# Kernel optimization log

Measured on AMD Instinct MI355X. Metric: run time of the kernel, lower is better.

## Reference

```python
import jax, jax.numpy as jnp
import numpy as np

N = 50000        # nodes
E = 800000       # edges
F_IN = 32        # float features (x also carries 1 trailing cell-id column)
CELL_DIM = 16
NUM_CELLS = 854
C = 64           # out_channels
H0, H1 = 2, 1    # heads schedule for num_layers=2 -> [2, 1]
D_IN = F_IN + CELL_DIM  # 48, GAT input dim after cell embedding concat
NEG_SLOPE = 0.2  # PyG GATConv default negative_slope


def setup_inputs() -> dict:
    key = jax.random.key(0)
    ks = jax.random.split(key, 14)
    base = jax.random.normal(ks[0], (N, F_IN), jnp.float32)
    cell_ids = jax.random.randint(ks[1], (N,), 0, NUM_CELLS)
    x = jnp.concatenate([base, cell_ids.astype(jnp.float32)[:, None]], axis=1)
    edge_index = jax.random.randint(ks[2], (2, E), 0, N, dtype=jnp.int32)
    s = lambda f: 1.0 / np.sqrt(f)
    emb = jax.random.normal(ks[3], (NUM_CELLS, CELL_DIM), jnp.float32)
    W0 = jax.random.normal(ks[4], (D_IN, H0 * C), jnp.float32) * s(D_IN)
    a_src0 = jax.random.normal(ks[5], (H0, C), jnp.float32) * s(C)
    a_dst0 = jax.random.normal(ks[6], (H0, C), jnp.float32) * s(C)
    b0 = jnp.zeros((C,), jnp.float32)
    ln_g = jnp.ones((C,), jnp.float32)
    ln_b = jnp.zeros((C,), jnp.float32)
    W1 = jax.random.normal(ks[7], (C, H1 * C), jnp.float32) * s(C)
    a_src1 = jax.random.normal(ks[8], (H1, C), jnp.float32) * s(C)
    a_dst1 = jax.random.normal(ks[9], (H1, C), jnp.float32) * s(C)
    b1 = jnp.zeros((C,), jnp.float32)
    return {"x": x, "edge_index": edge_index, "emb": emb,
            "W0": W0, "a_src0": a_src0, "a_dst0": a_dst0, "b0": b0,
            "ln_g": ln_g, "ln_b": ln_b,
            "W1": W1, "a_src1": a_src1, "a_dst1": a_dst1, "b1": b1}


def gat_layer(h_in, src, dst, W, a_src, a_dst, b, heads):
    # h_in: [N, D]; src/dst: [E'] (self-loops already appended)
    h = (h_in @ W).reshape(N, heads, C)                 # [N, H, C]
    alpha_s = jnp.einsum('nhc,hc->nh', h, a_src)        # [N, H]
    alpha_d = jnp.einsum('nhc,hc->nh', h, a_dst)
    e = jax.nn.leaky_relu(alpha_s[src] + alpha_d[dst], NEG_SLOPE)  # [E', H]
    # segment softmax over incoming edges of each dst node
    m = jax.ops.segment_max(e, dst, num_segments=N)     # [N, H]
    ex = jnp.exp(e - m[dst])
    denom = jax.ops.segment_sum(ex, dst, num_segments=N)
    alpha = ex / denom[dst]                             # [E', H]
    msg = h[src] * alpha[:, :, None]                    # [E', H, C]
    out = jax.ops.segment_sum(msg, dst, num_segments=N) # [N, H, C]
    return out.mean(axis=1) + b                         # concat=False -> mean over heads


def layer_norm(x, g, b):
    mu = x.mean(-1, keepdims=True)
    var = ((x - mu) ** 2).mean(-1, keepdims=True)
    return (x - mu) * jax.lax.rsqrt(var + 1e-5) * g + b


def reference(x, edge_index, emb, W0, a_src0, a_dst0, b0, ln_g, ln_b,
              W1, a_src1, a_dst1, b1):
    base = x[:, :-1]
    cell_ids = x[:, -1].astype(jnp.int32)
    h = jnp.concatenate([base, emb[cell_ids]], axis=1)  # [N, 48]
    # add self-loops (PyG GATConv default add_self_loops=True)
    loop = jnp.arange(N, dtype=edge_index.dtype)
    src = jnp.concatenate([edge_index[0], loop])
    dst = jnp.concatenate([edge_index[1], loop])
    h = gat_layer(h, src, dst, W0, a_src0, a_dst0, b0, H0)
    h = jax.nn.elu(layer_norm(h, ln_g, ln_b))           # dropout is identity at eval
    h = gat_layer(h, src, dst, W1, a_src1, a_dst1, b1, H1)
    return h
```

## Files before the change

kernel.cpp:

```cpp
#include <hip/hip_runtime.h>
#include <hip/hip_bf16.h>

#define N_NODES 50000
#define N_EDGES 800000
#define E_TOT 850000
#define F_IN 32
#define CELL_DIM 16
#define D_IN 48
#define X_STRIDE 33
#define NUM_CELLS 854
#define NEG_SLOPE 0.2f
#define NODE0_BLOCKS 1024
#define MERGE_BLOCKS 1563
#define EDGE_BLOCKS 3125
#define NXCD 8
#define BWX 16
#define W 24
#define NP 12

typedef unsigned int uint;
typedef unsigned short ushort;

static __device__ __forceinline__ uint f2b(float f) {
  uint x = __float_as_uint(f);
  return (x + 0x7fffu + ((x >> 16) & 1u)) >> 16;
}
static __device__ __forceinline__ float b2f_lo(uint w) { return __uint_as_float(w << 16); }
static __device__ __forceinline__ float b2f_hi(uint w) { return __uint_as_float(w & 0xffff0000u); }
static __device__ __forceinline__ float lrelu(float e) { return fmaxf(e, NEG_SLOPE * e); }


__global__ __launch_bounds__(256) void k_nb(const float* __restrict__ x,
                                            const float* __restrict__ emb,
                                            const float* __restrict__ W0,
                                            const float* __restrict__ asrc,
                                            const float* __restrict__ adst,
                                            const int* __restrict__ ei,
                                            ushort* __restrict__ h0u,
                                            float* __restrict__ as0, float* __restrict__ ad0,
                                            int* __restrict__ cnt, ushort* __restrict__ bkt) {
  int tid = threadIdx.x;
  if (blockIdx.x >= NODE0_BLOCKS) {
    int e = (blockIdx.x - NODE0_BLOCKS) * 256 + tid;
    if (e < N_EDGES) {
      uint xcc;
      asm volatile("s_getreg_b32 %0, hwreg(HW_REG_XCC_ID)" : "=s"(xcc));
      xcc &= (NXCD - 1);
      int s = ei[e], d = ei[N_EDGES + e];
      int p = atomicAdd(&cnt[xcc * N_NODES + d], 1);
      if (p < BWX) bkt[(xcc * N_NODES + d) * BWX + p] = (ushort)s;
    }
    return;
  }
  __shared__ float hin[8][48];
  int lane = tid & 63, wid = tid >> 6;
  int h = wid & 1;
  int q = wid >> 1;
  float w0r[D_IN];
#pragma unroll
  for (int k = 0; k < D_IN; ++k) w0r[k] = W0[k * 128 + h * 64 + lane];
  float av_s = asrc[h * 64 + lane], av_d = adst[h * 64 + lane];

  for (int g = blockIdx.x; g < N_NODES / 8; g += NODE0_BLOCKS) {
    int nb = g * 8;
#pragma unroll
    for (int j = 0; j < 2; ++j) {
      int loc = 2 * wid + j;
      int n = nb + loc;
      float t = 0.f;
      if (lane < 33) t = x[n * X_STRIDE + lane];
      int cid = (int)__shfl(t, 32, 64);
      cid = cid < 0 ? 0 : (cid >= NUM_CELLS ? NUM_CELLS - 1 : cid);
      if (lane >= 32 && lane < 48) t = emb[cid * CELL_DIM + (lane - 32)];
      if (lane < 48) hin[loc][lane] = t;
    }
    __syncthreads();
#pragma unroll
    for (int j = 0; j < 4; ++j) {
      int loc = 4 * q + j;
      int n = nb + loc;
      const float4* hp = (const float4*)hin[loc];
      float acc = 0.f;
#pragma unroll
      for (int k4 = 0; k4 < 12; ++k4) {
        float4 hh = hp[k4];
        acc = fmaf(hh.x, w0r[4 * k4 + 0], acc);
        acc = fmaf(hh.y, w0r[4 * k4 + 1], acc);
        acc = fmaf(hh.z, w0r[4 * k4 + 2], acc);
        acc = fmaf(hh.w, w0r[4 * k4 + 3], acc);
      }
      h0u[(n * 64 + lane) * 2 + h] = (ushort)f2b(acc);
      float sa = acc * av_s, sd = acc * av_d;
#pragma unroll
      for (int o = 32; o >= 1; o >>= 1) {
        sa += __shfl_xor(sa, o, 64);
        sd += __shfl_xor(sd, o, 64);
      }
      if (lane == 0) {
        as0[n * 2 + h] = sa;
        ad0[n * 2 + h] = sd;
      }
    }
    __syncthreads();
  }
}


__global__ __launch_bounds__(256) void k_merge(const int* __restrict__ cnt,
                                               const ushort* __restrict__ bkt,
                                               const float2* __restrict__ as0v,
                                               const float2* __restrict__ ad0v,
                                               int* __restrict__ galloc,
                                               int2* __restrict__ meta,
                                               ushort* __restrict__ srcs,
                                               uint* __restrict__ wts) {
  __shared__ int gpre[32];
  __shared__ int bbase;
  int tid = threadIdx.x;
  int grp = tid >> 3;
  int n = blockIdx.x * 32 + grp;
  bool alive = (n < N_NODES);
  int xg = tid & 7;
  int cx = alive ? min(cnt[xg * N_NODES + n], BWX) : 0;
  int sc = cx;
#pragma unroll
  for (int o = 1; o < 8; o <<= 1) {
    int t = __shfl_up(sc, o, 64);
    if ((tid & 7) >= o) sc += t;
  }
  int total = __shfl(sc, (tid & 63) | 7, 64);
  int items = alive ? total + 1 : 0;
  if (xg == 7) gpre[grp] = items;
  __syncthreads();
  if (tid < 32) {
    int v = gpre[tid];
    int s = v;
#pragma unroll
    for (int o = 1; o < 32; o <<= 1) {
      int t = __shfl_up(s, o, 64);
      if (tid >= o) s += t;
    }
    gpre[tid] = s - v;
    if (tid == 31) bbase = atomicAdd(galloc, s);
  }
  __syncthreads();
  if (!alive) return;
  int start = bbase + gpre[grp];
  int base = start + (sc - cx);
  float2 ad = ad0v[n];
  const ushort* src = bkt + (xg * N_NODES + n) * BWX;
  for (int k = 0; k < cx; ++k) {
    uint s = src[k];
    float2 a = as0v[s];
    uint wp = f2b(__expf(lrelu(a.x + ad.x))) | (f2b(__expf(lrelu(a.y + ad.y))) << 16);
    srcs[base + k] = (ushort)s;
    wts[base + k] = wp;
  }
  if (xg == 7) {
    float2 a = as0v[n];
    uint wp = f2b(__expf(lrelu(a.x + ad.x))) | (f2b(__expf(lrelu(a.y + ad.y))) << 16);
    srcs[start + total] = (ushort)n;
    wts[start + total] = wp;
    meta[n] = make_int2(start, items);
  }
}


__global__ __launch_bounds__(256) void k_agg0(const int2* __restrict__ meta,
                                              const ushort* __restrict__ srcs,
                                              const uint* __restrict__ wts,
                                              const uint* __restrict__ h0p,
                                              const float* __restrict__ b0,
                                              const float* __restrict__ lng,
                                              const float* __restrict__ lnb,
                                              const float* __restrict__ W1,
                                              const float* __restrict__ asrc1,
                                              const float* __restrict__ adst1,
                                              ushort* __restrict__ h1b,
                                              float* __restrict__ as1, float* __restrict__ ad1) {
  __shared__ uint gbuf[4][W * 64];
  __shared__ float yb[4][64];
  int tid = threadIdx.x;
  int lane = tid & 63, wl = tid >> 6;
  int n = blockIdx.x * 4 + wl;
  int2 mt = meta[n];
  int i0 = mt.x, i1 = mt.x + mt.y;
  float acc0 = 0.f, acc1 = 0.f, den0 = 0.f, den1 = 0.f;
  uint* gb = gbuf[wl];

  for (int w0 = i0; w0 < i1; w0 += W) {
    int idx = w0 + lane;
    uint s = 0u, wy = 0u;
    if (lane < W && idx < i1) {
      s = (uint)srcs[idx];
      wy = wts[idx];
    }
#pragma unroll
    for (int j = 0; j < W; ++j) {
      uint sx = (uint)__builtin_amdgcn_readlane((int)s, j);
      __builtin_amdgcn_global_load_lds((const uint*)(h0p + sx * 64u + (uint)lane),
                                       gb + j * 64, 4, 0, 0);
    }
    asm volatile("s_waitcnt vmcnt(0)" ::: "memory");
    __builtin_amdgcn_sched_barrier(0);
#pragma unroll
    for (int j = 0; j < W; ++j) {
      uint wyj = (uint)__builtin_amdgcn_readlane((int)wy, j);
      uint h = gb[j * 64 + lane];
      float w;
      w = b2f_lo(wyj); acc0 += w * b2f_lo(h); den0 += w;
      w = b2f_hi(wyj); acc1 += w * b2f_hi(h); den1 += w;
    }
    asm volatile("s_waitcnt lgkmcnt(0)" ::: "memory");
    __builtin_amdgcn_sched_barrier(0);
  }

  float v = 0.5f * (acc0 / den0 + acc1 / den1) + b0[lane];
  float mu = v;
#pragma unroll
  for (int o = 32; o >= 1; o >>= 1) mu += __shfl_xor(mu, o, 64);
  mu *= (1.0f / 64.0f);
  float d = v - mu;
  float vr = d * d;
#pragma unroll
  for (int o = 32; o >= 1; o >>= 1) vr += __shfl_xor(vr, o, 64);
  vr *= (1.0f / 64.0f);
  float y = d * rsqrtf(vr + 1e-5f) * lng[lane] + lnb[lane];
  y = y > 0.f ? y : expm1f(y);
  yb[wl][lane] = y;
  const float4* yp = (const float4*)yb[wl];
  float q0 = 0.f, q1 = 0.f, q2 = 0.f, q3 = 0.f;
#pragma unroll
  for (int k4 = 0; k4 < 16; ++k4) {
    float4 yy = yp[k4];
    q0 = fmaf(yy.x, W1[(4 * k4 + 0) * 64 + lane], q0);
    q1 = fmaf(yy.y, W1[(4 * k4 + 1) * 64 + lane], q1);
    q2 = fmaf(yy.z, W1[(4 * k4 + 2) * 64 + lane], q2);
    q3 = fmaf(yy.w, W1[(4 * k4 + 3) * 64 + lane], q3);
  }
  float h1v = (q0 + q1) + (q2 + q3);
  h1b[n * 64 + lane] = (ushort)f2b(h1v);
  float sa = h1v * asrc1[lane];
  float sdv = h1v * adst1[lane];
#pragma unroll
  for (int o = 32; o >= 1; o >>= 1) {
    sa += __shfl_xor(sa, o, 64);
    sdv += __shfl_xor(sdv, o, 64);
  }
  if (lane == 0) {
    as1[n] = sa;
    ad1[n] = sdv;
  }
}


__global__ __launch_bounds__(256) void k_agg1(const int2* __restrict__ meta,
                                              const ushort* __restrict__ srcs,
                                              const ushort* __restrict__ h1b,
                                              const float* __restrict__ as1,
                                              const float* __restrict__ ad1,
                                              const float* __restrict__ b1,
                                              float* __restrict__ out) {
  __shared__ uint gbuf[4][NP * 64];
  int tid = threadIdx.x;
  int lane = tid & 63, wl = tid >> 6;
  int n = blockIdx.x * 4 + wl;
  int2 mt = meta[n];
  int i0 = mt.x, i1 = mt.x + mt.y;
  float adv = ad1[n];
  float acc = 0.f, den = 0.f;
  uint* gb = gbuf[wl];
  const ushort* gbs = (const ushort*)gb;
  uint hl = lane & 31;
  int half = lane >> 5;

  for (int w0 = i0; w0 < i1; w0 += W) {
    int idx = w0 + lane;
    uint s = 0u;
    float wv = 0.f;
    if (lane < W && idx < i1) {
      s = (uint)srcs[idx];
      wv = __expf(lrelu(as1[s] + adv));
    }
#pragma unroll
    for (int j = 0; j < NP; ++j) {
      uint sxA = (uint)__builtin_amdgcn_readlane((int)s, 2 * j);
      uint sxB = (uint)__builtin_amdgcn_readlane((int)s, 2 * j + 1);
      uint sx2 = half ? sxB : sxA;
      __builtin_amdgcn_global_load_lds((const uint*)(h1b + sx2 * 64u) + hl,
                                       gb + j * 64, 4, 0, 0);
    }
    asm volatile("s_waitcnt vmcnt(0)" ::: "memory");
    __builtin_amdgcn_sched_barrier(0);
#pragma unroll
    for (int j = 0; j < NP; ++j) {
      float wA = __uint_as_float(
          (uint)__builtin_amdgcn_readlane((int)__float_as_uint(wv), 2 * j));
      float wB = __uint_as_float(
          (uint)__builtin_amdgcn_readlane((int)__float_as_uint(wv), 2 * j + 1));
      uint hA = (uint)gbs[j * 128 + lane];
      uint hB = (uint)gbs[j * 128 + 64 + lane];
      acc = fmaf(wA, __uint_as_float(hA << 16), acc);
      den += wA;
      acc = fmaf(wB, __uint_as_float(hB << 16), acc);
      den += wB;
    }
    asm volatile("s_waitcnt lgkmcnt(0)" ::: "memory");
    __builtin_amdgcn_sched_barrier(0);
  }
  out[n * 64 + lane] = acc / den + b1[lane];
}


extern "C" void kernel_launch(void* const* d_in, const int* in_sizes, int n_in,
                              void* d_out, int out_size, void* d_ws, size_t ws_size,
                              hipStream_t stream) {
  const float* x    = (const float*)d_in[0];
  const int*   ei   = (const int*)d_in[1];
  const float* emb  = (const float*)d_in[2];
  const float* W0   = (const float*)d_in[3];
  const float* as0w = (const float*)d_in[4];
  const float* ad0w = (const float*)d_in[5];
  const float* b0   = (const float*)d_in[6];
  const float* lng  = (const float*)d_in[7];
  const float* lnb  = (const float*)d_in[8];
  const float* W1   = (const float*)d_in[9];
  const float* as1w = (const float*)d_in[10];
  const float* ad1w = (const float*)d_in[11];
  const float* b1   = (const float*)d_in[12];
  float* out = (float*)d_out;

  ushort* bkt    = (ushort*)d_ws;
  ushort* h1b    = (ushort*)d_ws;
  int*    cnt    = (int*)((char*)d_ws + (size_t)NXCD * N_NODES * BWX * 2);
  int*    galloc = cnt + NXCD * N_NODES;
  float*  as1    = (float*)cnt;
  float*  ad1    = as1 + N_NODES;
  int2*   meta   = (int2*)(galloc + 2);
  ushort* srcs   = (ushort*)(meta + N_NODES);
  uint*   wts    = (uint*)(srcs + E_TOT);
  float*  as0    = (float*)(wts + E_TOT);
  float*  ad0    = as0 + N_NODES * 2;
  uint*   h0p    = (uint*)(ad0 + N_NODES * 2);

  hipMemsetAsync(cnt, 0, (NXCD * N_NODES + 2) * sizeof(int), stream);
  k_nb<<<NODE0_BLOCKS + EDGE_BLOCKS, 256, 0, stream>>>(x, emb, W0, as0w, ad0w, ei,
                                                       (ushort*)h0p, as0, ad0, cnt, bkt);
  k_merge<<<MERGE_BLOCKS, 256, 0, stream>>>(cnt, bkt, (const float2*)as0,
                                            (const float2*)ad0, galloc, meta, srcs, wts);
  k_agg0<<<N_NODES / 4, 256, 0, stream>>>(meta, srcs, wts, h0p, b0, lng, lnb, W1,
                                          as1w, ad1w, h1b, as1, ad1);
  k_agg1<<<N_NODES / 4, 256, 0, stream>>>(meta, srcs, h1b, as1, ad1, b1, out);
}
```

Measured before the change: 240.0 us.

## Precompute layer-1 edge weights in separate edge-parallel kernel packed with source ids

Adds a k_merge output of per-edge destination ids and a new edge-parallel kernel k_wts1. That kernel computes the layer-1 attention weight exp(lrelu(as1[s]+ad1[d])) for every edge and packs it as bf16 with the 16-bit source id into one 32-bit record. k_agg1 then reads a single packed record per edge instead of a source id plus a dependent as1 gather and exp. This moves latency-bound dependent gathers off the aggregation critical path into a fully parallel pass. The cost is an extra kernel launch, an extra edge array write and read, and layer-1 weights rounded to bf16.

```diff
diff --git a/kernel.cpp b/kernel.cpp
--- a/kernel.cpp
+++ b/kernel.cpp
@@ -13,6 +13,7 @@
 #define NODE0_BLOCKS 1024
 #define MERGE_BLOCKS 1563
 #define EDGE_BLOCKS 3125
+#define WTS1_BLOCKS 3321
 #define NXCD 8
 #define BWX 16
 #define W 24
@@ -113,6 +114,7 @@
                                                int* __restrict__ galloc,
                                                int2* __restrict__ meta,
                                                ushort* __restrict__ srcs,
+                                               ushort* __restrict__ dsts,
                                                uint* __restrict__ wts) {
   __shared__ int gpre[32];
   __shared__ int bbase;
@@ -154,12 +156,14 @@
     float2 a = as0v[s];
     uint wp = f2b(__expf(lrelu(a.x + ad.x))) | (f2b(__expf(lrelu(a.y + ad.y))) << 16);
     srcs[base + k] = (ushort)s;
+    dsts[base + k] = (ushort)n;
     wts[base + k] = wp;
   }
   if (xg == 7) {
     float2 a = as0v[n];
     uint wp = f2b(__expf(lrelu(a.x + ad.x))) | (f2b(__expf(lrelu(a.y + ad.y))) << 16);
     srcs[start + total] = (ushort)n;
+    dsts[start + total] = (ushort)n;
     wts[start + total] = wp;
     meta[n] = make_int2(start, items);
   }
@@ -254,11 +258,22 @@
 }
 
 
-__global__ __launch_bounds__(256) void k_agg1(const int2* __restrict__ meta,
-                                              const ushort* __restrict__ srcs,
-                                              const ushort* __restrict__ h1b,
+__global__ __launch_bounds__(256) void k_wts1(const ushort* __restrict__ srcs,
+                                              const ushort* __restrict__ dsts,
                                               const float* __restrict__ as1,
                                               const float* __restrict__ ad1,
+                                              uint* __restrict__ rec32) {
+  int e = blockIdx.x * 256 + threadIdx.x;
+  if (e >= E_TOT) return;
+  uint s = srcs[e], d = dsts[e];
+  float w = __expf(lrelu(as1[s] + ad1[d]));
+  rec32[e] = s | (f2b(w) << 16);
+}
+
+
+__global__ __launch_bounds__(256) void k_agg1(const int2* __restrict__ meta,
+                                              const uint* __restrict__ rec32,
+                                              const ushort* __restrict__ h1b,
                                               const float* __restrict__ b1,
                                               float* __restrict__ out) {
   __shared__ uint gbuf[4][NP * 64];
@@ -267,7 +282,6 @@
   int n = blockIdx.x * 4 + wl;
   int2 mt = meta[n];
   int i0 = mt.x, i1 = mt.x + mt.y;
-  float adv = ad1[n];
   float acc = 0.f, den = 0.f;
   uint* gb = gbuf[wl];
   const ushort* gbs = (const ushort*)gb;
@@ -276,17 +290,13 @@
 
   for (int w0 = i0; w0 < i1; w0 += W) {
     int idx = w0 + lane;
-    uint s = 0u;
-    float wv = 0.f;
-    if (lane < W && idx < i1) {
-      s = (uint)srcs[idx];
-      wv = __expf(lrelu(as1[s] + adv));
-    }
+    uint rec = 0u;
+    if (lane < W && idx < i1) rec = rec32[idx];
 #pragma unroll
     for (int j = 0; j < NP; ++j) {
-      uint sxA = (uint)__builtin_amdgcn_readlane((int)s, 2 * j);
-      uint sxB = (uint)__builtin_amdgcn_readlane((int)s, 2 * j + 1);
-      uint sx2 = half ? sxB : sxA;
+      uint rA = (uint)__builtin_amdgcn_readlane((int)rec, 2 * j);
+      uint rB = (uint)__builtin_amdgcn_readlane((int)rec, 2 * j + 1);
+      uint sx2 = (half ? rB : rA) & 0xffffu;
       __builtin_amdgcn_global_load_lds((const uint*)(h1b + sx2 * 64u) + hl,
                                        gb + j * 64, 4, 0, 0);
     }
@@ -294,10 +304,8 @@
     __builtin_amdgcn_sched_barrier(0);
 #pragma unroll
     for (int j = 0; j < NP; ++j) {
-      float wA = __uint_as_float(
-          (uint)__builtin_amdgcn_readlane((int)__float_as_uint(wv), 2 * j));
-      float wB = __uint_as_float(
-          (uint)__builtin_amdgcn_readlane((int)__float_as_uint(wv), 2 * j + 1));
+      float wA = b2f_hi((uint)__builtin_amdgcn_readlane((int)rec, 2 * j));
+      float wB = b2f_hi((uint)__builtin_amdgcn_readlane((int)rec, 2 * j + 1));
       uint hA = (uint)gbs[j * 128 + lane];
       uint hB = (uint)gbs[j * 128 + 64 + lane];
       acc = fmaf(wA, __uint_as_float(hA << 16), acc);
@@ -332,13 +340,15 @@
 
   ushort* bkt    = (ushort*)d_ws;
   ushort* h1b    = (ushort*)d_ws;
+  uint*   rec32  = (uint*)((char*)d_ws + (size_t)N_NODES * 64 * 2);
   int*    cnt    = (int*)((char*)d_ws + (size_t)NXCD * N_NODES * BWX * 2);
   int*    galloc = cnt + NXCD * N_NODES;
   float*  as1    = (float*)cnt;
   float*  ad1    = as1 + N_NODES;
   int2*   meta   = (int2*)(galloc + 2);
   ushort* srcs   = (ushort*)(meta + N_NODES);
-  uint*   wts    = (uint*)(srcs + E_TOT);
+  ushort* dsts   = srcs + E_TOT;
+  uint*   wts    = (uint*)(dsts + E_TOT);
   float*  as0    = (float*)(wts + E_TOT);
   float*  ad0    = as0 + N_NODES * 2;
   uint*   h0p    = (uint*)(ad0 + N_NODES * 2);
@@ -347,8 +357,9 @@
   k_nb<<<NODE0_BLOCKS + EDGE_BLOCKS, 256, 0, stream>>>(x, emb, W0, as0w, ad0w, ei,
                                                        (ushort*)h0p, as0, ad0, cnt, bkt);
   k_merge<<<MERGE_BLOCKS, 256, 0, stream>>>(cnt, bkt, (const float2*)as0,
-                                            (const float2*)ad0, galloc, meta, srcs, wts);
+                                            (const float2*)ad0, galloc, meta, srcs, dsts, wts);
   k_agg0<<<N_NODES / 4, 256, 0, stream>>>(meta, srcs, wts, h0p, b0, lng, lnb, W1,
                                           as1w, ad1w, h1b, as1, ad1);
-  k_agg1<<<N_NODES / 4, 256, 0, stream>>>(meta, srcs, h1b, as1, ad1, b1, out);
-}
+  k_wts1<<<WTS1_BLOCKS, 256, 0, stream>>>(srcs, dsts, as1, ad1, rec32);
+  k_agg1<<<N_NODES / 4, 256, 0, stream>>>(meta, rec32, h1b, b1, out);
+}
```

After: 240.8 us. No clear change (+0.4%).
